# Kernel tuning notes

Hardware: AMD Instinct MI355X
Metric: run time of the kernel (lower is better)

## Reference

```python
import jax, jax.numpy as jnp
import numpy as np

B, C, H, W = 8, 256, 128, 128
HEADS = 16
HEADC = C // HEADS  # 16
EPS = 1e-5


def setup_inputs() -> dict:
    key = jax.random.key(0)
    k1, k2 = jax.random.split(key)
    x = jax.random.normal(k1, (B, C, H, W), dtype=jnp.float32)
    w_qkv = jax.random.normal(k2, (3 * C, C), dtype=jnp.float32) * (1.0 / np.sqrt(C))
    b_qkv = jnp.zeros((3 * C,), dtype=jnp.float32)
    kln_w = jnp.ones((HEADS, HEADC), dtype=jnp.float32)
    kln_b = jnp.zeros((HEADS, HEADC), dtype=jnp.float32)
    vln_w = jnp.ones((HEADS, HEADC), dtype=jnp.float32)
    vln_b = jnp.zeros((HEADS, HEADC), dtype=jnp.float32)
    return {"x": x, "w_qkv": w_qkv, "b_qkv": b_qkv,
            "kln_w": kln_w, "kln_b": kln_b, "vln_w": vln_w, "vln_b": vln_b}


def _layernorm(x, w, b):
    # torch-style: unbiased std (ddof=1), divides by (std + eps), over last dim
    mean = jnp.mean(x, axis=-1, keepdims=True)
    std = jnp.std(x, axis=-1, keepdims=True, ddof=1)
    return (x - mean) / (std + EPS) * w + b


def reference(x, w_qkv, b_qkv, kln_w, kln_b, vln_w, vln_b):
    b, c, h, w = x.shape
    n = h * w
    # 1x1 conv == per-pixel matmul over channels
    qkv = jnp.einsum('bchw,oc->bhwo', x, w_qkv) + b_qkv  # (B,H,W,3C)
    qkv = qkv.reshape(b, n, HEADS, -1)                   # (B,N,16,3*headc)
    q, k, v = jnp.split(qkv, 3, axis=-1)                 # each (B,N,16,headc)
    k = _layernorm(k, kln_w, kln_b)
    v = _layernorm(v, vln_w, vln_b)
    # linear (Galerkin) attention: kv = k^T v / N, out = q @ kv
    kv = jnp.einsum('bnhd,bnhe->bhde', k, v) / n         # (B,16,headc,headc)
    out = jnp.einsum('bnhd,bhde->bnhe', q, kv)           # (B,N,16,headc)
    out = out.reshape(b, h, w, c).transpose(0, 3, 1, 2)  # (B,C,H,W)
    return out
```

## Files before the change

### kernel.cpp

```cpp
#include <hip/hip_runtime.h>

typedef unsigned short u16;
typedef unsigned int u32;
typedef __attribute__((ext_vector_type(8))) short short8;
typedef __attribute__((ext_vector_type(4))) float f32x4;

#define NPIX 16384
#define LNEPS 1e-5f

__device__ __forceinline__ float bf2f(u16 u) {
  union { u32 i; float f; } x; x.i = ((u32)u) << 16; return x.f;
}
__device__ __forceinline__ u16 f2bf(float f) {
  union { float f; u32 i; } x; x.f = f;
  u32 r = x.i + 0x7fffu + ((x.i >> 16) & 1u);
  return (u16)(r >> 16);
}
__device__ __forceinline__ void gload_lds16(const void* g, void* l) {
  __builtin_amdgcn_global_load_lds((__attribute__((address_space(1))) void*)(g),
                                   (__attribute__((address_space(3))) void*)(l),
                                   16, 0, 0);
}

__global__ __launch_bounds__(256) void k_detect(const u16* __restrict__ x,
                                                int* __restrict__ flag) {
  float mx = 0.f;
  for (int i = threadIdx.x; i < 4096; i += 256) {
    float v = fabsf(bf2f(x[2 * i]));
    if (v == v) mx = fmaxf(mx, v);
  }
  for (int m = 1; m < 64; m <<= 1) mx = fmaxf(mx, __shfl_xor(mx, m));
  __shared__ float wmax[4];
  if ((threadIdx.x & 63) == 0) wmax[threadIdx.x >> 6] = mx;
  __syncthreads();
  if (threadIdx.x == 0) {
    float m2 = fmaxf(fmaxf(wmax[0], wmax[1]), fmaxf(wmax[2], wmax[3]));
    flag[0] = (m2 > 1e5f) ? 1 : 0;
  }
}

__global__ __launch_bounds__(256) void k_wconv(
    const void* __restrict__ w, const void* __restrict__ bq,
    const void* __restrict__ klw, const void* __restrict__ klb,
    const void* __restrict__ vlw, const void* __restrict__ vlb,
    u16* __restrict__ wkv, u16* __restrict__ wq,
    float* __restrict__ bias_kv, float* __restrict__ lnw_kv,
    float* __restrict__ lnb_kv, float* __restrict__ bq_q,
    const int* __restrict__ flag) {
  const int i = blockIdx.x * 256 + threadIdx.x;
  const bool f32 = flag[0] != 0;
  auto getf = [&](const void* p, int j) -> float {
    return f32 ? ((const float*)p)[j] : bf2f(((const u16*)p)[j]);
  };
  if (i < 131072) {
    int o = i >> 8, c = i & 255;
    int h = o >> 5, tt = (o >> 4) & 1, d = o & 15;
    wkv[i] = f2bf(getf(w, (h * 48 + 16 + tt * 16 + d) * 256 + c));
  } else if (i < 196608) {
    int j = i - 131072; int r = j >> 8, c = j & 255;
    wq[j] = f2bf(getf(w, ((r >> 4) * 48 + (r & 15)) * 256 + c));
  } else if (i < 198400) {
    int j = i - 196608;
    if (j < 512) {
      int h = j >> 5, tt = (j >> 4) & 1, d = j & 15;
      bias_kv[j] = getf(bq, h * 48 + 16 + tt * 16 + d);
    } else if (j < 1024) {
      int o = j - 512; int h = o >> 5, tt = (o >> 4) & 1, d = o & 15;
      lnw_kv[o] = getf(tt ? vlw : klw, h * 16 + d);
    } else if (j < 1536) {
      int o = j - 1024; int h = o >> 5, tt = (o >> 4) & 1, d = o & 15;
      lnb_kv[o] = getf(tt ? vlb : klb, h * 16 + d);
    } else {
      int r = j - 1536;
      bq_q[r] = getf(bq, (r >> 4) * 48 + (r & 15));
    }
  }
}

__global__ __launch_bounds__(256, 2) void k_gemm1(
    const void* __restrict__ xin, const u16* __restrict__ wkv,
    const float* __restrict__ bias_kv, const float* __restrict__ lnw_kv,
    const float* __restrict__ lnb_kv, float* __restrict__ kvpart,
    const int* __restrict__ flag) {
  __shared__ u16 wlds[256][32];
  __shared__ u16 xlds[32][128];
  __shared__ u16 klds[128][132];
  __shared__ float bls[256], wls[256], lls[256];
  __shared__ float tmp[2][256];

  const int t = threadIdx.x;
  const int hg = blockIdx.x & 1;
  const int pc = (blockIdx.x >> 1) & 127;
  const int b  = blockIdx.x >> 8;
  const int p0 = pc * 128;
  const int wv = t >> 6, lane = t & 63, quad = lane >> 4, l16 = lane & 15;
  const bool f32 = flag[0] != 0;

  bls[t] = bias_kv[hg * 256 + t];
  wls[t] = lnw_kv[hg * 256 + t];
  lls[t] = lnb_kv[hg * 256 + t];

  f32x4 acc[16][2];
#pragma unroll
  for (int ms = 0; ms < 16; ++ms) {
    acc[ms][0] = (f32x4){0.f, 0.f, 0.f, 0.f};
    acc[ms][1] = (f32x4){0.f, 0.f, 0.f, 0.f};
  }

  const u16* wsrc = wkv + ((size_t)(hg * 256 + (t >> 2)) * 256 + (t & 3) * 8);

  for (int ks = 0; ks < 8; ++ks) {
#pragma unroll
    for (int i = 0; i < 4; ++i)
      gload_lds16(wsrc + ks * 32 + (size_t)i * 64 * 256,
                  &wlds[i * 64 + (t >> 2)][(t & 3) * 8]);
    if (!f32) {
      const u16* xs0 = (const u16*)xin +
          ((size_t)(b * 256 + ks * 32 + (t >> 4)) * NPIX + p0 + (t & 15) * 8);
#pragma unroll
      for (int i = 0; i < 2; ++i)
        gload_lds16(xs0 + (size_t)i * 16 * NPIX,
                    &xlds[i * 16 + (t >> 4)][(t & 15) * 8]);
    } else {
      const float* xf = (const float*)xin +
          ((size_t)(b * 256 + ks * 32 + (t >> 3)) * NPIX + p0 + (t & 7) * 16);
      float4 v0 = *(const float4*)xf;
      float4 v1 = *(const float4*)(xf + 4);
      float4 v2 = *(const float4*)(xf + 8);
      float4 v3 = *(const float4*)(xf + 12);
      uint4 q0, q1;
      q0.x = (u32)f2bf(v0.x) | ((u32)f2bf(v0.y) << 16);
      q0.y = (u32)f2bf(v0.z) | ((u32)f2bf(v0.w) << 16);
      q0.z = (u32)f2bf(v1.x) | ((u32)f2bf(v1.y) << 16);
      q0.w = (u32)f2bf(v1.z) | ((u32)f2bf(v1.w) << 16);
      q1.x = (u32)f2bf(v2.x) | ((u32)f2bf(v2.y) << 16);
      q1.y = (u32)f2bf(v2.z) | ((u32)f2bf(v2.w) << 16);
      q1.z = (u32)f2bf(v3.x) | ((u32)f2bf(v3.y) << 16);
      q1.w = (u32)f2bf(v3.z) | ((u32)f2bf(v3.w) << 16);
      *(uint4*)&xlds[t >> 3][(t & 7) * 16] = q0;
      *(uint4*)&xlds[t >> 3][(t & 7) * 16 + 8] = q1;
    }
    __syncthreads();
    short8 bfr[2];
#pragma unroll
    for (int ns = 0; ns < 2; ++ns) {
      short8 bv;
#pragma unroll
      for (int j = 0; j < 8; ++j)
        bv[j] = (short)xlds[quad * 8 + j][wv * 32 + ns * 16 + l16];
      bfr[ns] = bv;
    }
#pragma unroll
    for (int ms = 0; ms < 16; ++ms) {
      short8 av = *(const short8*)&wlds[ms * 16 + l16][quad * 8];
      acc[ms][0] = __builtin_amdgcn_mfma_f32_16x16x32_bf16(av, bfr[0], acc[ms][0], 0, 0, 0);
      acc[ms][1] = __builtin_amdgcn_mfma_f32_16x16x32_bf16(av, bfr[1], acc[ms][1], 0, 0, 0);
    }
    __syncthreads();
  }

#pragma unroll
  for (int p = 0; p < 4; ++p) {
    __syncthreads();
#pragma unroll
    for (int j = 0; j < 4; ++j) {
      const int ms = p * 4 + j;
      const int cb = (j >> 1) * 64 + (j & 1) * 16;
      float4 bi = *(const float4*)&bls[ms * 16 + quad * 4];
      float4 lw = *(const float4*)&wls[ms * 16 + quad * 4];
      float4 lb = *(const float4*)&lls[ms * 16 + quad * 4];
      float biv[4] = {bi.x, bi.y, bi.z, bi.w};
      float lwv[4] = {lw.x, lw.y, lw.z, lw.w};
      float lbv[4] = {lb.x, lb.y, lb.z, lb.w};
#pragma unroll
      for (int ns = 0; ns < 2; ++ns) {
        const int px = wv * 32 + ns * 16 + l16;
        float x0[4];
#pragma unroll
        for (int r = 0; r < 4; ++r) x0[r] = acc[ms][ns][r] + biv[r];
        float s1 = x0[0] + x0[1] + x0[2] + x0[3];
        s1 += __shfl_xor(s1, 16);
        s1 += __shfl_xor(s1, 32);
        float mean = s1 * (1.0f / 16.0f);
        float dv[4];
#pragma unroll
        for (int r = 0; r < 4; ++r) dv[r] = x0[r] - mean;
        float s2 = dv[0]*dv[0] + dv[1]*dv[1] + dv[2]*dv[2] + dv[3]*dv[3];
        s2 += __shfl_xor(s2, 16);
        s2 += __shfl_xor(s2, 32);
        float var = s2 * (1.0f / 15.0f);
        float rstd = 1.0f / (sqrtf(var) + LNEPS);
        u16 hi[4], lo[4];
#pragma unroll
        for (int r = 0; r < 4; ++r) {
          float kn = dv[r] * rstd * lwv[r] + lbv[r];
          hi[r] = f2bf(kn);
          lo[r] = f2bf(kn - bf2f(hi[r]));
        }
        uint2 ph, pl;
        ph.x = (u32)hi[0] | ((u32)hi[1] << 16);
        ph.y = (u32)hi[2] | ((u32)hi[3] << 16);
        pl.x = (u32)lo[0] | ((u32)lo[1] << 16);
        pl.y = (u32)lo[2] | ((u32)lo[3] << 16);
        *(uint2*)&klds[px][cb + quad * 4] = ph;
        *(uint2*)&klds[px][cb + 32 + quad * 4] = pl;
      }
    }
    __syncthreads();
    const int hh = wv >> 1, combo = wv & 1, cb = hh * 64;
    f32x4 kva = (f32x4){0.f, 0.f, 0.f, 0.f};
    if (combo == 0) {
#pragma unroll
      for (int px2 = 0; px2 < 4; ++px2) {
        short8 av, bv;
#pragma unroll
        for (int jj = 0; jj < 8; ++jj) {
          av[jj] = (short)klds[px2 * 32 + quad * 8 + jj][cb + l16];
          bv[jj] = (short)klds[px2 * 32 + quad * 8 + jj][cb + 16 + l16];
        }
        kva = __builtin_amdgcn_mfma_f32_16x16x32_bf16(av, bv, kva, 0, 0, 0);
      }
    } else {
#pragma unroll
      for (int px2 = 0; px2 < 4; ++px2) {
        short8 ah, al, vh, vl;
#pragma unroll
        for (int jj = 0; jj < 8; ++jj) {
          const int px = px2 * 32 + quad * 8 + jj;
          ah[jj] = (short)klds[px][cb + l16];
          vh[jj] = (short)klds[px][cb + 16 + l16];
          al[jj] = (short)klds[px][cb + 32 + l16];
          vl[jj] = (short)klds[px][cb + 48 + l16];
        }
        kva = __builtin_amdgcn_mfma_f32_16x16x32_bf16(ah, vl, kva, 0, 0, 0);
        kva = __builtin_amdgcn_mfma_f32_16x16x32_bf16(al, vh, kva, 0, 0, 0);
      }
    }
    __syncthreads();
    if (combo) {
#pragma unroll
      for (int r = 0; r < 4; ++r) tmp[hh][(quad * 4 + r) * 16 + l16] = kva[r];
    }
    __syncthreads();
    if (!combo) {
      float* kvp = kvpart +
          ((size_t)(((b * 128 + pc) * 2 + hg) * 8 + (p * 2 + hh)) << 8);
#pragma unroll
      for (int r = 0; r < 4; ++r) {
        const int idx = (quad * 4 + r) * 16 + l16;
        kvp[idx] = kva[r] + tmp[hh][idx];
      }
    }
  }
}

__global__ __launch_bounds__(256) void k_reduce(const float* __restrict__ kvpart,
                                                float* __restrict__ kvg) {
  const int t = threadIdx.x;
  const int b = blockIdx.x >> 4, h = blockIdx.x & 15;
  const int hg = h >> 3, hl = h & 7;
  const float* src = kvpart + ((size_t)((b * 128 * 2 + hg) * 8 + hl) << 8) + t;
  float s = 0.f;
  for (int pc = 0; pc < 128; ++pc)
    s += src[(size_t)pc * (2 * 8 * 256)];
  kvg[((size_t)blockIdx.x << 8) + t] = s * (1.0f / 16384.0f);
}

__global__ __launch_bounds__(256) void k_fold(const u16* __restrict__ wq,
                                              const float* __restrict__ bq_q,
                                              const float* __restrict__ kvg,
                                              u16* __restrict__ whi,
                                              u16* __restrict__ wlo,
                                              float* __restrict__ beff) {
  __shared__ float kvs[256];
  __shared__ float qb[16];
  const int t = threadIdx.x;
  const int b = blockIdx.x >> 4, h = blockIdx.x & 15;
  kvs[t] = kvg[((size_t)blockIdx.x << 8) + t];
  if (t < 16) qb[t] = bq_q[h * 16 + t];
  __syncthreads();
  const int e = t >> 4, c0 = (t & 15) * 16;
  float o[16];
#pragma unroll
  for (int c = 0; c < 16; ++c) o[c] = 0.f;
  for (int d = 0; d < 16; ++d) {
    float kv_de = kvs[d * 16 + e];
    const u16* wr = wq + (size_t)(h * 16 + d) * 256 + c0;
#pragma unroll
    for (int c = 0; c < 16; ++c) o[c] = fmaf(bf2f(wr[c]), kv_de, o[c]);
  }
  const size_t wbase = (size_t)(b * 256 + h * 16 + e) * 256 + c0;
#pragma unroll
  for (int c = 0; c < 16; ++c) {
    u16 hi = f2bf(o[c]);
    whi[wbase + c] = hi;
    wlo[wbase + c] = f2bf(o[c] - bf2f(hi));
  }
  if (t < 16) {
    float s = 0.f;
    for (int d = 0; d < 16; ++d) s += qb[d] * kvs[d * 16 + t];
    beff[b * 256 + h * 16 + t] = s;
  }
}

__global__ __launch_bounds__(256, 2) void k_gemm2(
    const void* __restrict__ xin, const u16* __restrict__ whi,
    const u16* __restrict__ wlo, const float* __restrict__ beff,
    void* __restrict__ outv, const int* __restrict__ flag) {
  __shared__ u16 wldh[256][32];
  __shared__ u16 wldl[256][32];
  __shared__ u16 xlds[32][128];
  __shared__ float bls[256];

  const int t = threadIdx.x;
  const int pc = blockIdx.x & 127;
  const int b  = blockIdx.x >> 7;
  const int p0 = pc * 128;
  const int wv = t >> 6, lane = t & 63, quad = lane >> 4, l16 = lane & 15;
  const bool f32 = flag[0] != 0;

  bls[t] = beff[b * 256 + t];

  f32x4 acc[16][2];
#pragma unroll
  for (int ms = 0; ms < 16; ++ms) {
    acc[ms][0] = (f32x4){0.f, 0.f, 0.f, 0.f};
    acc[ms][1] = (f32x4){0.f, 0.f, 0.f, 0.f};
  }

  const size_t woff = ((size_t)(b * 256 + (t >> 2)) * 256 + (t & 3) * 8);
  const u16* wsrch = whi + woff;
  const u16* wsrcl = wlo + woff;

  for (int ks = 0; ks < 8; ++ks) {
#pragma unroll
    for (int i = 0; i < 4; ++i) {
      gload_lds16(wsrch + ks * 32 + (size_t)i * 64 * 256,
                  &wldh[i * 64 + (t >> 2)][(t & 3) * 8]);
      gload_lds16(wsrcl + ks * 32 + (size_t)i * 64 * 256,
                  &wldl[i * 64 + (t >> 2)][(t & 3) * 8]);
    }
    if (!f32) {
      const u16* xs0 = (const u16*)xin +
          ((size_t)(b * 256 + ks * 32 + (t >> 4)) * NPIX + p0 + (t & 15) * 8);
#pragma unroll
      for (int i = 0; i < 2; ++i)
        gload_lds16(xs0 + (size_t)i * 16 * NPIX,
                    &xlds[i * 16 + (t >> 4)][(t & 15) * 8]);
    } else {
      const float* xf = (const float*)xin +
          ((size_t)(b * 256 + ks * 32 + (t >> 3)) * NPIX + p0 + (t & 7) * 16);
      float4 v0 = *(const float4*)xf;
      float4 v1 = *(const float4*)(xf + 4);
      float4 v2 = *(const float4*)(xf + 8);
      float4 v3 = *(const float4*)(xf + 12);
      uint4 q0, q1;
      q0.x = (u32)f2bf(v0.x) | ((u32)f2bf(v0.y) << 16);
      q0.y = (u32)f2bf(v0.z) | ((u32)f2bf(v0.w) << 16);
      q0.z = (u32)f2bf(v1.x) | ((u32)f2bf(v1.y) << 16);
      q0.w = (u32)f2bf(v1.z) | ((u32)f2bf(v1.w) << 16);
      q1.x = (u32)f2bf(v2.x) | ((u32)f2bf(v2.y) << 16);
      q1.y = (u32)f2bf(v2.z) | ((u32)f2bf(v2.w) << 16);
      q1.z = (u32)f2bf(v3.x) | ((u32)f2bf(v3.y) << 16);
      q1.w = (u32)f2bf(v3.z) | ((u32)f2bf(v3.w) << 16);
      *(uint4*)&xlds[t >> 3][(t & 7) * 16] = q0;
      *(uint4*)&xlds[t >> 3][(t & 7) * 16 + 8] = q1;
    }
    __syncthreads();
    short8 bfr[2];
#pragma unroll
    for (int ns = 0; ns < 2; ++ns) {
      short8 bv;
#pragma unroll
      for (int j = 0; j < 8; ++j)
        bv[j] = (short)xlds[quad * 8 + j][wv * 32 + ns * 16 + l16];
      bfr[ns] = bv;
    }
#pragma unroll
    for (int ms = 0; ms < 16; ++ms) {
      short8 avh = *(const short8*)&wldh[ms * 16 + l16][quad * 8];
      short8 avl = *(const short8*)&wldl[ms * 16 + l16][quad * 8];
      acc[ms][0] = __builtin_amdgcn_mfma_f32_16x16x32_bf16(avh, bfr[0], acc[ms][0], 0, 0, 0);
      acc[ms][0] = __builtin_amdgcn_mfma_f32_16x16x32_bf16(avl, bfr[0], acc[ms][0], 0, 0, 0);
      acc[ms][1] = __builtin_amdgcn_mfma_f32_16x16x32_bf16(avh, bfr[1], acc[ms][1], 0, 0, 0);
      acc[ms][1] = __builtin_amdgcn_mfma_f32_16x16x32_bf16(avl, bfr[1], acc[ms][1], 0, 0, 0);
    }
    __syncthreads();
  }

  const size_t obase = (size_t)b * 256 * NPIX + p0;
#pragma unroll
  for (int ms = 0; ms < 16; ++ms) {
    float4 be = *(const float4*)&bls[ms * 16 + quad * 4];
    float bev[4] = {be.x, be.y, be.z, be.w};
#pragma unroll
    for (int ns = 0; ns < 2; ++ns) {
      const int px = wv * 32 + ns * 16 + l16;
#pragma unroll
      for (int r = 0; r < 4; ++r) {
        const int o = ms * 16 + quad * 4 + r;
        float val = acc[ms][ns][r] + bev[r];
        if (f32) ((float*)outv)[obase + (size_t)o * NPIX + px] = val;
        else ((u16*)outv)[obase + (size_t)o * NPIX + px] = f2bf(val);
      }
    }
  }
}

extern "C" void kernel_launch(void* const* d_in, const int* in_sizes, int n_in,
                              void* d_out, int out_size, void* d_ws, size_t ws_size,
                              hipStream_t stream) {
  (void)in_sizes; (void)n_in; (void)out_size; (void)ws_size;
  char* ws = (char*)d_ws;
  u16* wkv       = (u16*)(ws + 0);
  u16* wq        = (u16*)(ws + 262144);
  u16* weff_hi   = (u16*)(ws + 393216);
  u16* weff_lo   = (u16*)(ws + 1441792);
  float* kvg     = (float*)(ws + 2490368);
  float* bias_kv = (float*)(ws + 2621440);
  float* lnw_kv  = (float*)(ws + 2623488);
  float* lnb_kv  = (float*)(ws + 2625536);
  float* bq_q    = (float*)(ws + 2627584);
  float* beff    = (float*)(ws + 2628608);
  int* flag      = (int*)(ws + 2636800);
  float* kvpart  = (float*)(ws + 4194304);

  k_detect<<<1, 256, 0, stream>>>((const u16*)d_in[0], flag);
  k_wconv<<<775, 256, 0, stream>>>(d_in[1], d_in[2], d_in[3], d_in[4], d_in[5],
                                   d_in[6], wkv, wq, bias_kv, lnw_kv, lnb_kv,
                                   bq_q, flag);
  k_gemm1<<<2048, 256, 0, stream>>>(d_in[0], wkv, bias_kv, lnw_kv, lnb_kv,
                                    kvpart, flag);
  k_reduce<<<128, 256, 0, stream>>>(kvpart, kvg);
  k_fold<<<128, 256, 0, stream>>>(wq, bq_q, kvg, weff_hi, weff_lo, beff);
  k_gemm2<<<1024, 256, 0, stream>>>(d_in[0], weff_hi, weff_lo, beff, d_out, flag);
}
```

Before: 377.9 us.

## Double-buffer GEMM LDS tiles, swizzle layouts, and split waves across 512-thread blocks

Both GEMM kernels move from 256 to 512 threads per block, so each wave holds half the output rows (8 accumulator tiles instead of 16), which lowers register pressure. The x and weight tiles are double-buffered so the next k-slice loads while MFMAs run on the current one. XOR swizzles are added to the LDS layouts to cut bank conflicts, LDS buffers are aliased to fit a larger klds, and block IDs are remapped for XCD locality. The cost is more LDS per block, extra sync complexity, and the need for the remapped head indexing in the LN and kv stage to stay correct.

After: 371.3 us. No clear change (-1.8%).

```diff
diff --git a/kernel.cpp b/kernel.cpp
--- a/kernel.cpp
+++ b/kernel.cpp
@@ -20,6 +20,14 @@
   __builtin_amdgcn_global_load_lds((__attribute__((address_space(1))) void*)(g),
                                    (__attribute__((address_space(3))) void*)(l),
                                    16, 0, 0);
+}
+__device__ __forceinline__ uint4 pack8(float4 a, float4 b) {
+  uint4 q;
+  q.x = (u32)f2bf(a.x) | ((u32)f2bf(a.y) << 16);
+  q.y = (u32)f2bf(a.z) | ((u32)f2bf(a.w) << 16);
+  q.z = (u32)f2bf(b.x) | ((u32)f2bf(b.y) << 16);
+  q.w = (u32)f2bf(b.z) | ((u32)f2bf(b.w) << 16);
+  return q;
 }
 
 __global__ __launch_bounds__(256) void k_detect(const u16* __restrict__ x,
@@ -77,107 +85,126 @@
   }
 }
 
-__global__ __launch_bounds__(256, 2) void k_gemm1(
+__global__ __launch_bounds__(512, 4) void k_gemm1(
     const void* __restrict__ xin, const u16* __restrict__ wkv,
     const float* __restrict__ bias_kv, const float* __restrict__ lnw_kv,
     const float* __restrict__ lnb_kv, float* __restrict__ kvpart,
     const int* __restrict__ flag) {
-  __shared__ u16 wlds[256][32];
-  __shared__ u16 xlds[32][128];
-  __shared__ u16 klds[128][132];
-  __shared__ float bls[256], wls[256], lls[256];
-  __shared__ float tmp[2][256];
+  __shared__ alignas(16) char shraw[73728];
+  u16 (*wlds)[256][32] = (u16 (*)[256][32])shraw;
+  u16 (*xlds)[32][128] = (u16 (*)[32][128])(shraw + 32768);
+  u16 (*klds)[260]     = (u16 (*)[260])shraw;
+  float* bls = (float*)(shraw + 66560);
+  float* wls = bls + 256;
+  float* lls = bls + 512;
+  float (*tmp)[256] = (float (*)[256])(shraw + 69632);
 
   const int t = threadIdx.x;
-  const int hg = blockIdx.x & 1;
-  const int pc = (blockIdx.x >> 1) & 127;
-  const int b  = blockIdx.x >> 8;
+  const int lbid = ((blockIdx.x & 7) << 8) + (blockIdx.x >> 3);
+  const int hg = lbid & 1;
+  const int pc = (lbid >> 1) & 127;
+  const int b  = lbid >> 8;
   const int p0 = pc * 128;
   const int wv = t >> 6, lane = t & 63, quad = lane >> 4, l16 = lane & 15;
+  const int hl = wv & 1, pxq = wv >> 1;
   const bool f32 = flag[0] != 0;
 
-  bls[t] = bias_kv[hg * 256 + t];
-  wls[t] = lnw_kv[hg * 256 + t];
-  lls[t] = lnb_kv[hg * 256 + t];
-
-  f32x4 acc[16][2];
-#pragma unroll
-  for (int ms = 0; ms < 16; ++ms) {
+  if (t < 256) {
+    bls[t] = bias_kv[hg * 256 + t];
+    wls[t] = lnw_kv[hg * 256 + t];
+    lls[t] = lnb_kv[hg * 256 + t];
+  }
+
+  f32x4 acc[8][2];
+#pragma unroll
+  for (int ms = 0; ms < 8; ++ms) {
     acc[ms][0] = (f32x4){0.f, 0.f, 0.f, 0.f};
     acc[ms][1] = (f32x4){0.f, 0.f, 0.f, 0.f};
   }
 
-  const u16* wsrc = wkv + ((size_t)(hg * 256 + (t >> 2)) * 256 + (t & 3) * 8);
+  const int wrow = t >> 2;
+  const int wcs  = t & 3;
+  const int wks  = (wcs ^ ((t >> 3) & 3)) * 8;
+  const u16* wsrc = wkv + ((size_t)(hg * 256 + wrow) * 256 + wks);
+
+  const int xrow = t >> 4;
+  const int xg   = (t & 15) ^ ((xrow >> 3) << 1);
+  const u16* xsrc_bf = (const u16*)xin +
+      ((size_t)(b * 256 + xrow) * NPIX + p0 + xg * 8);
+  const float* xsrc_f = (const float*)xin +
+      ((size_t)(b * 256 + xrow) * NPIX + p0 + xg * 8);
+
+  gload_lds16(wsrc, &wlds[0][wrow][wcs * 8]);
+  gload_lds16(wsrc + (size_t)128 * 256, &wlds[0][128 + wrow][wcs * 8]);
+  if (!f32) {
+    gload_lds16(xsrc_bf, &xlds[0][xrow][(t & 15) * 8]);
+  } else {
+    float4 a = *(const float4*)xsrc_f;
+    float4 c = *(const float4*)(xsrc_f + 4);
+    *(uint4*)&xlds[0][xrow][(t & 15) * 8] = pack8(a, c);
+  }
+  __syncthreads();
 
   for (int ks = 0; ks < 8; ++ks) {
-#pragma unroll
-    for (int i = 0; i < 4; ++i)
-      gload_lds16(wsrc + ks * 32 + (size_t)i * 64 * 256,
-                  &wlds[i * 64 + (t >> 2)][(t & 3) * 8]);
-    if (!f32) {
-      const u16* xs0 = (const u16*)xin +
-          ((size_t)(b * 256 + ks * 32 + (t >> 4)) * NPIX + p0 + (t & 15) * 8);
-#pragma unroll
-      for (int i = 0; i < 2; ++i)
-        gload_lds16(xs0 + (size_t)i * 16 * NPIX,
-                    &xlds[i * 16 + (t >> 4)][(t & 15) * 8]);
-    } else {
-      const float* xf = (const float*)xin +
-          ((size_t)(b * 256 + ks * 32 + (t >> 3)) * NPIX + p0 + (t & 7) * 16);
-      float4 v0 = *(const float4*)xf;
-      float4 v1 = *(const float4*)(xf + 4);
-      float4 v2 = *(const float4*)(xf + 8);
-      float4 v3 = *(const float4*)(xf + 12);
-      uint4 q0, q1;
-      q0.x = (u32)f2bf(v0.x) | ((u32)f2bf(v0.y) << 16);
-      q0.y = (u32)f2bf(v0.z) | ((u32)f2bf(v0.w) << 16);
-      q0.z = (u32)f2bf(v1.x) | ((u32)f2bf(v1.y) << 16);
-      q0.w = (u32)f2bf(v1.z) | ((u32)f2bf(v1.w) << 16);
-      q1.x = (u32)f2bf(v2.x) | ((u32)f2bf(v2.y) << 16);
-      q1.y = (u32)f2bf(v2.z) | ((u32)f2bf(v2.w) << 16);
-      q1.z = (u32)f2bf(v3.x) | ((u32)f2bf(v3.y) << 16);
-      q1.w = (u32)f2bf(v3.z) | ((u32)f2bf(v3.w) << 16);
-      *(uint4*)&xlds[t >> 3][(t & 7) * 16] = q0;
-      *(uint4*)&xlds[t >> 3][(t & 7) * 16 + 8] = q1;
-    }
-    __syncthreads();
+    const int cur = ks & 1, nxt = cur ^ 1;
+    const bool more = ks < 7;
+    float4 v0, v1;
+    if (more) {
+      const u16* ws = wsrc + (ks + 1) * 32;
+      gload_lds16(ws, &wlds[nxt][wrow][wcs * 8]);
+      gload_lds16(ws + (size_t)128 * 256, &wlds[nxt][128 + wrow][wcs * 8]);
+      if (!f32) {
+        gload_lds16(xsrc_bf + (size_t)(ks + 1) * 32 * NPIX,
+                    &xlds[nxt][xrow][(t & 15) * 8]);
+      } else {
+        const float* xf = xsrc_f + (size_t)(ks + 1) * 32 * NPIX;
+        v0 = *(const float4*)xf;
+        v1 = *(const float4*)(xf + 4);
+      }
+    }
     short8 bfr[2];
 #pragma unroll
     for (int ns = 0; ns < 2; ++ns) {
+      const int pxn = pxq * 32 + ns * 16 + l16;
+      const int cs8 = ((((pxn >> 3) ^ (quad << 1)) << 3) + (pxn & 7));
       short8 bv;
 #pragma unroll
       for (int j = 0; j < 8; ++j)
-        bv[j] = (short)xlds[quad * 8 + j][wv * 32 + ns * 16 + l16];
+        bv[j] = (short)xlds[cur][quad * 8 + j][cs8];
       bfr[ns] = bv;
     }
 #pragma unroll
-    for (int ms = 0; ms < 16; ++ms) {
-      short8 av = *(const short8*)&wlds[ms * 16 + l16][quad * 8];
+    for (int ms = 0; ms < 8; ++ms) {
+      const int row = hl * 128 + ms * 16 + l16;
+      short8 av = *(const short8*)&wlds[cur][row][(quad ^ ((l16 >> 1) & 3)) * 8];
       acc[ms][0] = __builtin_amdgcn_mfma_f32_16x16x32_bf16(av, bfr[0], acc[ms][0], 0, 0, 0);
       acc[ms][1] = __builtin_amdgcn_mfma_f32_16x16x32_bf16(av, bfr[1], acc[ms][1], 0, 0, 0);
     }
-    __syncthreads();
-  }
-
-#pragma unroll
-  for (int p = 0; p < 4; ++p) {
+    if (more && f32)
+      *(uint4*)&xlds[nxt][xrow][(t & 15) * 8] = pack8(v0, v1);
+    __syncthreads();
+  }
+
+#pragma unroll
+  for (int p = 0; p < 2; ++p) {
     __syncthreads();
 #pragma unroll
     for (int j = 0; j < 4; ++j) {
-      const int ms = p * 4 + j;
-      const int cb = (j >> 1) * 64 + (j & 1) * 16;
-      float4 bi = *(const float4*)&bls[ms * 16 + quad * 4];
-      float4 lw = *(const float4*)&wls[ms * 16 + quad * 4];
-      float4 lb = *(const float4*)&lls[ms * 16 + quad * 4];
+      const int msl = p * 4 + j;
+      const int slot = (j >> 1) | (hl << 1);
+      const int cb = slot * 64 + (j & 1) * 16;
+      float4 bi = *(const float4*)&bls[hl * 128 + msl * 16 + quad * 4];
+      float4 lw = *(const float4*)&wls[hl * 128 + msl * 16 + quad * 4];
+      float4 lb = *(const float4*)&lls[hl * 128 + msl * 16 + quad * 4];
       float biv[4] = {bi.x, bi.y, bi.z, bi.w};
       float lwv[4] = {lw.x, lw.y, lw.z, lw.w};
       float lbv[4] = {lb.x, lb.y, lb.z, lb.w};
 #pragma unroll
       for (int ns = 0; ns < 2; ++ns) {
-        const int px = wv * 32 + ns * 16 + l16;
+        const int px = pxq * 32 + ns * 16 + l16;
         float x0[4];
 #pragma unroll
-        for (int r = 0; r < 4; ++r) x0[r] = acc[ms][ns][r] + biv[r];
+        for (int r = 0; r < 4; ++r) x0[r] = acc[msl][ns][r] + biv[r];
         float s1 = x0[0] + x0[1] + x0[2] + x0[3];
         s1 += __shfl_xor(s1, 16);
         s1 += __shfl_xor(s1, 32);
@@ -207,7 +234,8 @@
       }
     }
     __syncthreads();
-    const int hh = wv >> 1, combo = wv & 1, cb = hh * 64;
+    const int slot4 = wv >> 1, combo = wv & 1;
+    const int cb2 = slot4 * 64;
     f32x4 kva = (f32x4){0.f, 0.f, 0.f, 0.f};
     if (combo == 0) {
 #pragma unroll
@@ -215,8 +243,8 @@
         short8 av, bv;
 #pragma unroll
         for (int jj = 0; jj < 8; ++jj) {
-          av[jj] = (short)klds[px2 * 32 + quad * 8 + jj][cb + l16];
-          bv[jj] = (short)klds[px2 * 32 + quad * 8 + jj][cb + 16 + l16];
+          av[jj] = (short)klds[px2 * 32 + quad * 8 + jj][cb2 + l16];
+          bv[jj] = (short)klds[px2 * 32 + quad * 8 + jj][cb2 + 16 + l16];
         }
         kva = __builtin_amdgcn_mfma_f32_16x16x32_bf16(av, bv, kva, 0, 0, 0);
       }
@@ -227,10 +255,10 @@
 #pragma unroll
         for (int jj = 0; jj < 8; ++jj) {
           const int px = px2 * 32 + quad * 8 + jj;
-          ah[jj] = (short)klds[px][cb + l16];
-          vh[jj] = (short)klds[px][cb + 16 + l16];
-          al[jj] = (short)klds[px][cb + 32 + l16];
-          vl[jj] = (short)klds[px][cb + 48 + l16];
+          ah[jj] = (short)klds[px][cb2 + l16];
+          vh[jj] = (short)klds[px][cb2 + 16 + l16];
+          al[jj] = (short)klds[px][cb2 + 32 + l16];
+          vl[jj] = (short)klds[px][cb2 + 48 + l16];
         }
         kva = __builtin_amdgcn_mfma_f32_16x16x32_bf16(ah, vl, kva, 0, 0, 0);
         kva = __builtin_amdgcn_mfma_f32_16x16x32_bf16(al, vh, kva, 0, 0, 0);
@@ -239,16 +267,17 @@
     __syncthreads();
     if (combo) {
 #pragma unroll
-      for (int r = 0; r < 4; ++r) tmp[hh][(quad * 4 + r) * 16 + l16] = kva[r];
+      for (int r = 0; r < 4; ++r) tmp[slot4][(quad * 4 + r) * 16 + l16] = kva[r];
     }
     __syncthreads();
     if (!combo) {
+      const int h = (slot4 >> 1) * 4 + p * 2 + (slot4 & 1);
       float* kvp = kvpart +
-          ((size_t)(((b * 128 + pc) * 2 + hg) * 8 + (p * 2 + hh)) << 8);
+          ((size_t)(((b * 128 + pc) * 2 + hg) * 8 + h) << 8);
 #pragma unroll
       for (int r = 0; r < 4; ++r) {
         const int idx = (quad * 4 + r) * 16 + l16;
-        kvp[idx] = kva[r] + tmp[hh][idx];
+        kvp[idx] = kva[r] + tmp[slot4][idx];
       }
     }
   }
@@ -303,102 +332,120 @@
   }
 }
 
-__global__ __launch_bounds__(256, 2) void k_gemm2(
+__global__ __launch_bounds__(512, 4) void k_gemm2(
     const void* __restrict__ xin, const u16* __restrict__ whi,
     const u16* __restrict__ wlo, const float* __restrict__ beff,
     void* __restrict__ outv, const int* __restrict__ flag) {
-  __shared__ u16 wldh[256][32];
-  __shared__ u16 wldl[256][32];
-  __shared__ u16 xlds[32][128];
-  __shared__ float bls[256];
+  __shared__ alignas(16) char shraw[49152];
+  u16 (*wldh)[32] = (u16 (*)[32])shraw;
+  u16 (*wldl)[32] = (u16 (*)[32])(shraw + 16384);
+  u16 (*xlds)[32][128] = (u16 (*)[32][128])(shraw + 32768);
 
   const int t = threadIdx.x;
-  const int pc = blockIdx.x & 127;
-  const int b  = blockIdx.x >> 7;
+  const int lbid = ((blockIdx.x & 7) << 7) + (blockIdx.x >> 3);
+  const int pc = lbid & 127;
+  const int b  = lbid >> 7;
   const int p0 = pc * 128;
   const int wv = t >> 6, lane = t & 63, quad = lane >> 4, l16 = lane & 15;
+  const int hl = wv & 1, pxq = wv >> 1;
   const bool f32 = flag[0] != 0;
 
-  bls[t] = beff[b * 256 + t];
-
-  f32x4 acc[16][2];
-#pragma unroll
-  for (int ms = 0; ms < 16; ++ms) {
+  f32x4 acc[8][2];
+#pragma unroll
+  for (int ms = 0; ms < 8; ++ms) {
     acc[ms][0] = (f32x4){0.f, 0.f, 0.f, 0.f};
     acc[ms][1] = (f32x4){0.f, 0.f, 0.f, 0.f};
   }
 
-  const size_t woff = ((size_t)(b * 256 + (t >> 2)) * 256 + (t & 3) * 8);
-  const u16* wsrch = whi + woff;
-  const u16* wsrcl = wlo + woff;
+  const int wrow = t >> 2;
+  const int wcs  = t & 3;
+  const int wks  = (wcs ^ ((t >> 3) & 3)) * 8;
+  const size_t wbase = (size_t)(b * 256 + wrow) * 256 + wks;
+  const u16* wsrch = whi + wbase;
+  const u16* wsrcl = wlo + wbase;
+
+  const int xrow = t >> 4;
+  const int xg   = (t & 15) ^ ((xrow >> 3) << 1);
+  const u16* xsrc_bf = (const u16*)xin +
+      ((size_t)(b * 256 + xrow) * NPIX + p0 + xg * 8);
+  const float* xsrc_f = (const float*)xin +
+      ((size_t)(b * 256 + xrow) * NPIX + p0 + xg * 8);
+
+  gload_lds16(wsrch, &wldh[wrow][wcs * 8]);
+  gload_lds16(wsrch + (size_t)128 * 256, &wldh[128 + wrow][wcs * 8]);
+  gload_lds16(wsrcl, &wldl[wrow][wcs * 8]);
+  gload_lds16(wsrcl + (size_t)128 * 256, &wldl[128 + wrow][wcs * 8]);
+  if (!f32) {
+    gload_lds16(xsrc_bf, &xlds[0][xrow][(t & 15) * 8]);
+  } else {
+    float4 a = *(const float4*)xsrc_f;
+    float4 c = *(const float4*)(xsrc_f + 4);
+    *(uint4*)&xlds[0][xrow][(t & 15) * 8] = pack8(a, c);
+  }
+  __syncthreads();
 
   for (int ks = 0; ks < 8; ++ks) {
-#pragma unroll
-    for (int i = 0; i < 4; ++i) {
-      gload_lds16(wsrch + ks * 32 + (size_t)i * 64 * 256,
-                  &wldh[i * 64 + (t >> 2)][(t & 3) * 8]);
-      gload_lds16(wsrcl + ks * 32 + (size_t)i * 64 * 256,
-                  &wldl[i * 64 + (t >> 2)][(t & 3) * 8]);
-    }
-    if (!f32) {
-      const u16* xs0 = (const u16*)xin +
-          ((size_t)(b * 256 + ks * 32 + (t >> 4)) * NPIX + p0 + (t & 15) * 8);
-#pragma unroll
-      for (int i = 0; i < 2; ++i)
-        gload_lds16(xs0 + (size_t)i * 16 * NPIX,
-                    &xlds[i * 16 + (t >> 4)][(t & 15) * 8]);
-    } else {
-      const float* xf = (const float*)xin +
-          ((size_t)(b * 256 + ks * 32 + (t >> 3)) * NPIX + p0 + (t & 7) * 16);
-      float4 v0 = *(const float4*)xf;
-      float4 v1 = *(const float4*)(xf + 4);
-      float4 v2 = *(const float4*)(xf + 8);
-      float4 v3 = *(const float4*)(xf + 12);
-      uint4 q0, q1;
-      q0.x = (u32)f2bf(v0.x) | ((u32)f2bf(v0.y) << 16);
-      q0.y = (u32)f2bf(v0.z) | ((u32)f2bf(v0.w) << 16);
-      q0.z = (u32)f2bf(v1.x) | ((u32)f2bf(v1.y) << 16);
-      q0.w = (u32)f2bf(v1.z) | ((u32)f2bf(v1.w) << 16);
-      q1.x = (u32)f2bf(v2.x) | ((u32)f2bf(v2.y) << 16);
-      q1.y = (u32)f2bf(v2.z) | ((u32)f2bf(v2.w) << 16);
-      q1.z = (u32)f2bf(v3.x) | ((u32)f2bf(v3.y) << 16);
-      q1.w = (u32)f2bf(v3.z) | ((u32)f2bf(v3.w) << 16);
-      *(uint4*)&xlds[t >> 3][(t & 7) * 16] = q0;
-      *(uint4*)&xlds[t >> 3][(t & 7) * 16 + 8] = q1;
-    }
-    __syncthreads();
+    const int cur = ks & 1, nxt = cur ^ 1;
+    const bool more = ks < 7;
+    float4 v0, v1;
+    if (more) {
+      if (!f32) {
+        gload_lds16(xsrc_bf + (size_t)(ks + 1) * 32 * NPIX,
+                    &xlds[nxt][xrow][(t & 15) * 8]);
+      } else {
+        const float* xf = xsrc_f + (size_t)(ks + 1) * 32 * NPIX;
+        v0 = *(const float4*)xf;
+        v1 = *(const float4*)(xf + 4);
+      }
+    }
     short8 bfr[2];
 #pragma unroll
     for (int ns = 0; ns < 2; ++ns) {
+      const int pxn = pxq * 32 + ns * 16 + l16;
+      const int cs8 = ((((pxn >> 3) ^ (quad << 1)) << 3) + (pxn & 7));
       short8 bv;
 #pragma unroll
       for (int j = 0; j < 8; ++j)
-        bv[j] = (short)xlds[quad * 8 + j][wv * 32 + ns * 16 + l16];
+        bv[j] = (short)xlds[cur][quad * 8 + j][cs8];
       bfr[ns] = bv;
     }
 #pragma unroll
-    for (int ms = 0; ms < 16; ++ms) {
-      short8 avh = *(const short8*)&wldh[ms * 16 + l16][quad * 8];
-      short8 avl = *(const short8*)&wldl[ms * 16 + l16][quad * 8];
+    for (int ms = 0; ms < 8; ++ms) {
+      const int row = hl * 128 + ms * 16 + l16;
+      const int csw = (quad ^ ((l16 >> 1) & 3)) * 8;
+      short8 avh = *(const short8*)&wldh[row][csw];
+      short8 avl = *(const short8*)&wldl[row][csw];
       acc[ms][0] = __builtin_amdgcn_mfma_f32_16x16x32_bf16(avh, bfr[0], acc[ms][0], 0, 0, 0);
       acc[ms][0] = __builtin_amdgcn_mfma_f32_16x16x32_bf16(avl, bfr[0], acc[ms][0], 0, 0, 0);
       acc[ms][1] = __builtin_amdgcn_mfma_f32_16x16x32_bf16(avh, bfr[1], acc[ms][1], 0, 0, 0);
       acc[ms][1] = __builtin_amdgcn_mfma_f32_16x16x32_bf16(avl, bfr[1], acc[ms][1], 0, 0, 0);
     }
     __syncthreads();
+    if (more) {
+      const u16* wh = wsrch + (ks + 1) * 32;
+      const u16* wl = wsrcl + (ks + 1) * 32;
+      gload_lds16(wh, &wldh[wrow][wcs * 8]);
+      gload_lds16(wh + (size_t)128 * 256, &wldh[128 + wrow][wcs * 8]);
+      gload_lds16(wl, &wldl[wrow][wcs * 8]);
+      gload_lds16(wl + (size_t)128 * 256, &wldl[128 + wrow][wcs * 8]);
+      if (f32)
+        *(uint4*)&xlds[nxt][xrow][(t & 15) * 8] = pack8(v0, v1);
+      __syncthreads();
+    }
   }
 
   const size_t obase = (size_t)b * 256 * NPIX + p0;
 #pragma unroll
-  for (int ms = 0; ms < 16; ++ms) {
-    float4 be = *(const float4*)&bls[ms * 16 + quad * 4];
+  for (int ms = 0; ms < 8; ++ms) {
+    const int o0 = hl * 128 + ms * 16 + quad * 4;
+    float4 be = *(const float4*)&beff[b * 256 + o0];
     float bev[4] = {be.x, be.y, be.z, be.w};
 #pragma unroll
     for (int ns = 0; ns < 2; ++ns) {
-      const int px = wv * 32 + ns * 16 + l16;
+      const int px = pxq * 32 + ns * 16 + l16;
 #pragma unroll
       for (int r = 0; r < 4; ++r) {
-        const int o = ms * 16 + quad * 4 + r;
+        const int o = o0 + r;
         float val = acc[ms][ns][r] + bev[r];
         if (f32) ((float*)outv)[obase + (size_t)o * NPIX + px] = val;
         else ((u16*)outv)[obase + (size_t)o * NPIX + px] = f2bf(val);
@@ -429,9 +476,9 @@
   k_wconv<<<775, 256, 0, stream>>>(d_in[1], d_in[2], d_in[3], d_in[4], d_in[5],
                                    d_in[6], wkv, wq, bias_kv, lnw_kv, lnb_kv,
                                    bq_q, flag);
-  k_gemm1<<<2048, 256, 0, stream>>>(d_in[0], wkv, bias_kv, lnw_kv, lnb_kv,
+  k_gemm1<<<2048, 512, 0, stream>>>(d_in[0], wkv, bias_kv, lnw_kv, lnb_kv,
                                     kvpart, flag);
   k_reduce<<<128, 256, 0, stream>>>(kvpart, kvg);
   k_fold<<<128, 256, 0, stream>>>(wq, bq_q, kvg, weff_hi, weff_lo, beff);
-  k_gemm2<<<1024, 256, 0, stream>>>(d_in[0], weff_hi, weff_lo, beff, d_out, flag);
-}
+  k_gemm2<<<1024, 512, 0, stream>>>(d_in[0], weff_hi, weff_lo, beff, d_out, flag);
+}
```
